# Performance work log

Measured on AMD Instinct MI355X. Metric: run time of the kernel, lower is better.

Reference implementation:

```python
import jax, jax.numpy as jnp
import numpy as np

N_NODES = 50000
N_EDGES = 800000
HID = 256
HEADS = 4
HEAD_C = HID // HEADS  # 64
IN_CH = 16
OUT_CH = 4
NEG_SLOPE = 0.2  # PyG GATConv default LeakyReLU slope
LN_EPS = 1e-5


def setup_inputs() -> dict:
    key = jax.random.key(0)
    ks = jax.random.split(key, 12)
    s = 0.05
    return {
        "x": jax.random.normal(ks[0], (N_NODES, IN_CH), dtype=jnp.float32),
        "edge_index": jax.random.randint(ks[1], (2, N_EDGES), 0, N_NODES, dtype=jnp.int64),
        "w_in": jax.random.normal(ks[2], (IN_CH, HID), dtype=jnp.float32) * s,
        "b_in": jnp.zeros((HID,), dtype=jnp.float32),
        "w_gat": jax.random.normal(ks[3], (4, HID, HID), dtype=jnp.float32) * s,
        "att_src": jax.random.normal(ks[4], (4, HEADS, HEAD_C), dtype=jnp.float32) * s,
        "att_dst": jax.random.normal(ks[5], (4, HEADS, HEAD_C), dtype=jnp.float32) * s,
        "b_gat": jnp.zeros((4, HID), dtype=jnp.float32),
        "ln_scale": jnp.ones((4, HID), dtype=jnp.float32),
        "ln_bias": jnp.zeros((4, HID), dtype=jnp.float32),
        "w_out": jax.random.normal(ks[6], (HID, OUT_CH), dtype=jnp.float32) * s,
        "b_out": jnp.zeros((OUT_CH,), dtype=jnp.float32),
    }


def _gat_layer(x, src, dst, W, a_src, a_dst, bias, g, beta):
    """One GATConv(concat, heads=4) + LayerNorm + ELU. x:[N,HID]."""
    n = x.shape[0]
    h = (x @ W).reshape(n, HEADS, HEAD_C)                 # [N,H,C]
    a_s = jnp.einsum("nhc,hc->nh", h, a_src)              # [N,H]
    a_d = jnp.einsum("nhc,hc->nh", h, a_dst)              # [N,H]
    logits = jax.nn.leaky_relu(a_s[src] + a_d[dst], NEG_SLOPE)  # [E,H]
    # segment softmax over destination neighborhoods (self-loops ensure non-empty)
    m = jax.ops.segment_max(logits, dst, num_segments=n)
    e = jnp.exp(logits - m[dst])
    denom = jax.ops.segment_sum(e, dst, num_segments=n)
    alpha = e / (denom[dst] + 1e-16)                      # [E,H]
    msg = alpha[:, :, None] * h[src]                      # [E,H,C]
    out = jax.ops.segment_sum(msg, dst, num_segments=n).reshape(n, HID) + bias
    mu = out.mean(-1, keepdims=True)
    var = out.var(-1, keepdims=True)
    out = (out - mu) * jax.lax.rsqrt(var + LN_EPS) * g + beta
    return jax.nn.elu(out)


def reference(x, edge_index, w_in, b_in, w_gat, att_src, att_dst, b_gat,
              ln_scale, ln_bias, w_out, b_out):
    n = x.shape[0]
    # PyG GATConv adds self-loops by default
    loops = jnp.arange(n, dtype=edge_index.dtype)
    ei = jnp.concatenate([edge_index, jnp.stack([loops, loops])], axis=1)
    src, dst = ei[0], ei[1]

    x = x @ w_in + b_in                                   # input_proj
    h = x
    for l in (0, 1):
        h = _gat_layer(h, src, dst, w_gat[l], att_src[l], att_dst[l],
                       b_gat[l], ln_scale[l], ln_bias[l])
    x = x + h
    h = x
    for l in (2, 3):
        h = _gat_layer(h, src, dst, w_gat[l], att_src[l], att_dst[l],
                       b_gat[l], ln_scale[l], ln_bias[l])
    x = x + h
    return x @ w_out + b_out
```

## Files before the change

### kernel.cpp

```cpp
#include <hip/hip_runtime.h>
#include <math.h>

#define NN 50000
#define E0 800000
#define ET 850000
#define HID 256
#define INCH 16
#define MAXDEG 64

typedef _Float16 h8 __attribute__((ext_vector_type(8)));
typedef float f32x4 __attribute__((ext_vector_type(4)));

__global__ void scatter_pad_kernel(const int* __restrict__ ei, int* __restrict__ cursor,
                                   int* __restrict__ csr_pad) {
    int e = blockIdx.x * blockDim.x + threadIdx.x;
    if (e >= ET) return;
    int s, d;
    if (e < E0) { s = ei[e]; d = ei[E0 + e]; }
    else        { s = d = e - E0; }
    int pos = atomicAdd(&cursor[d], 1);
    if (pos < MAXDEG) csr_pad[(d << 6) + pos] = s;
}

__global__ __launch_bounds__(256) void wt_kernel(const float* __restrict__ w,
                                                 _Float16* __restrict__ wt) {
    int k = blockIdx.x, l = blockIdx.y, n = threadIdx.x;
    float v = w[((size_t)l * 256 + k) * 256 + n];
    wt[((size_t)l * 256 + n) * 256 + k] = (_Float16)v;
}

__global__ __launch_bounds__(256) void input_proj_kernel(
    const float* __restrict__ x, const float* __restrict__ w,
    const float* __restrict__ b, _Float16* __restrict__ outh) {
    int n = blockIdx.x, j = threadIdx.x;
    __shared__ float xs[INCH];
    if (j < INCH) xs[j] = x[n * INCH + j];
    __syncthreads();
    float acc = b[j];
#pragma unroll
    for (int k = 0; k < INCH; k++) acc += xs[k] * w[k * HID + j];
    outh[n * HID + j] = (_Float16)acc;
}

__global__ __launch_bounds__(512) void gemm_fused_kernel(
    const _Float16* __restrict__ A, const _Float16* __restrict__ BT,
    _Float16* __restrict__ H, const float* __restrict__ att_s,
    const float* __restrict__ att_d, float* __restrict__ AS, float* __restrict__ AD,
    int N) {
    int t = threadIdx.x;
    int wv = t >> 6, lane = t & 63;
    int rb = blockIdx.x * 128;
    int wr = (wv >> 2) * 64, wc = (wv & 3) * 64;
    int lm = lane & 15, lq = lane >> 4;
    f32x4 acc[4][4] = {};

    const _Float16* ap[4];
#pragma unroll
    for (int i = 0; i < 4; ++i) {
        int ra = rb + wr + i * 16 + lm;
        if (ra >= N) ra = N - 1;
        ap[i] = A + (size_t)ra * 256 + lq * 8;
    }
    const _Float16* bp[4];
#pragma unroll
    for (int j = 0; j < 4; ++j)
        bp[j] = BT + (size_t)(wc + j * 16 + lm) * 256 + lq * 8;

#pragma unroll 2
    for (int k0 = 0; k0 < 256; k0 += 32) {
        h8 af[4], bfr[4];
#pragma unroll
        for (int i = 0; i < 4; ++i) af[i] = *(const h8*)(ap[i] + k0);
#pragma unroll
        for (int j = 0; j < 4; ++j) bfr[j] = *(const h8*)(bp[j] + k0);
#pragma unroll
        for (int i = 0; i < 4; ++i)
#pragma unroll
            for (int j = 0; j < 4; ++j)
                acc[i][j] = __builtin_amdgcn_mfma_f32_16x16x32_f16(af[i], bfr[j], acc[i][j], 0, 0, 0);
    }

    int head = wv & 3;
    float sa[4], sd[4];
#pragma unroll
    for (int j = 0; j < 4; ++j) {
        sa[j] = att_s[head * 64 + j * 16 + lm];
        sd[j] = att_d[head * 64 + j * 16 + lm];
    }
#pragma unroll
    for (int i = 0; i < 4; ++i)
#pragma unroll
        for (int rr = 0; rr < 4; ++rr) {
            float vs = acc[i][0][rr] * sa[0] + acc[i][1][rr] * sa[1]
                     + acc[i][2][rr] * sa[2] + acc[i][3][rr] * sa[3];
            float vd = acc[i][0][rr] * sd[0] + acc[i][1][rr] * sd[1]
                     + acc[i][2][rr] * sd[2] + acc[i][3][rr] * sd[3];
#pragma unroll
            for (int o = 1; o <= 8; o <<= 1) {
                vs += __shfl_xor(vs, o, 64);
                vd += __shfl_xor(vd, o, 64);
            }
            int row = rb + wr + i * 16 + lq * 4 + rr;
            if (lm == 0 && row < N) {
                AS[row * 4 + head] = vs;
                AD[row * 4 + head] = vd;
            }
        }

#pragma unroll
    for (int i = 0; i < 4; ++i)
#pragma unroll
        for (int j = 0; j < 4; ++j) {
            int col = wc + j * 16 + lm;
#pragma unroll
            for (int rr = 0; rr < 4; ++rr) {
                int row = rb + wr + i * 16 + lq * 4 + rr;
                if (row < N) H[(size_t)row * 256 + col] = (_Float16)acc[i][j][rr];
            }
        }
}

__global__ __launch_bounds__(256) void agg_kernel(
    const _Float16* __restrict__ H, const float4* __restrict__ AS,
    const float4* __restrict__ AD,
    const int* __restrict__ cnt, const int* __restrict__ csr_pad,
    const float* __restrict__ bias, const float* __restrict__ g, const float* __restrict__ beta,
    const _Float16* __restrict__ res, _Float16* __restrict__ outh) {
    int t = threadIdx.x;
    int l32 = t & 31;
    int n = blockIdx.x * 8 + (t >> 5);
    int deg = cnt[n];
    if (deg > MAXDEG) deg = MAXDEG;
    int start = n << 6, end = start + deg;
    float4 adv = AD[n];
    int head = l32 >> 3;
    int c0 = l32 * 8;
    float advh = (head == 0) ? adv.x : (head == 1) ? adv.y : (head == 2) ? adv.z : adv.w;

    float acc[8] = {};
    float acc_e = 0.f;
#pragma unroll 4
    for (int i = start; i < end; ++i) {
        int s = csr_pad[i];
        const float* as = (const float*)&AS[s];
        float v = as[head] + advh;
        v = (v >= 0.f) ? v : 0.2f * v;
        float e = __expf(v);
        acc_e += e;
        h8 hv = *(const h8*)(H + (size_t)s * 256 + c0);
#pragma unroll
        for (int k = 0; k < 8; ++k) acc[k] += e * (float)hv[k];
    }
    float dinv = 1.f / (acc_e + 1e-16f);

    float val[8];
#pragma unroll
    for (int k = 0; k < 8; k += 4) {
        float4 bb = *(const float4*)(bias + c0 + k);
        val[k]     = acc[k]     * dinv + bb.x;
        val[k + 1] = acc[k + 1] * dinv + bb.y;
        val[k + 2] = acc[k + 2] * dinv + bb.z;
        val[k + 3] = acc[k + 3] * dinv + bb.w;
    }

    float s1 = 0.f, s2 = 0.f;
#pragma unroll
    for (int k = 0; k < 8; ++k) { s1 += val[k]; s2 += val[k] * val[k]; }
#pragma unroll
    for (int o = 16; o >= 1; o >>= 1) {
        s1 += __shfl_xor(s1, o, 64);
        s2 += __shfl_xor(s2, o, 64);
    }
    float mu = s1 * (1.f / 256.f);
    float var = s2 * (1.f / 256.f) - mu * mu;
    float rs = rsqrtf(var + 1e-5f);

    float y[8];
#pragma unroll
    for (int k = 0; k < 8; k += 4) {
        float4 g4 = *(const float4*)(g + c0 + k);
        float4 b4 = *(const float4*)(beta + c0 + k);
        y[k]     = (val[k]     - mu) * rs * g4.x + b4.x;
        y[k + 1] = (val[k + 1] - mu) * rs * g4.y + b4.y;
        y[k + 2] = (val[k + 2] - mu) * rs * g4.z + b4.z;
        y[k + 3] = (val[k + 3] - mu) * rs * g4.w + b4.w;
    }
#pragma unroll
    for (int k = 0; k < 8; ++k) y[k] = (y[k] > 0.f) ? y[k] : (__expf(y[k]) - 1.f);
    if (res) {
        h8 r0 = *(const h8*)(res + (size_t)n * 256 + c0);
#pragma unroll
        for (int k = 0; k < 8; ++k) y[k] += (float)r0[k];
    }
    h8 o0;
#pragma unroll
    for (int k = 0; k < 8; ++k) o0[k] = (_Float16)y[k];
    *(h8*)(outh + (size_t)n * 256 + c0) = o0;
}

__global__ __launch_bounds__(256) void out_proj_kernel(
    const _Float16* __restrict__ x, const float* __restrict__ w,
    const float* __restrict__ b, float* __restrict__ out, int n) {
    int tid = blockIdx.x * blockDim.x + threadIdx.x;
    int node = tid >> 6, lane = tid & 63;
    if (node >= n) return;
    const _Float16* xp = x + (size_t)node * HID + lane * 4;
    float x0 = (float)xp[0], x1 = (float)xp[1], x2 = (float)xp[2], x3 = (float)xp[3];
    const float4* wr = (const float4*)w;
    float4 w0 = wr[lane * 4 + 0];
    float4 w1 = wr[lane * 4 + 1];
    float4 w2 = wr[lane * 4 + 2];
    float4 w3 = wr[lane * 4 + 3];
    float o0 = x0 * w0.x + x1 * w1.x + x2 * w2.x + x3 * w3.x;
    float o1 = x0 * w0.y + x1 * w1.y + x2 * w2.y + x3 * w3.y;
    float o2 = x0 * w0.z + x1 * w1.z + x2 * w2.z + x3 * w3.z;
    float o3 = x0 * w0.w + x1 * w1.w + x2 * w2.w + x3 * w3.w;
#pragma unroll
    for (int o = 32; o >= 1; o >>= 1) {
        o0 += __shfl_down(o0, o, 64);
        o1 += __shfl_down(o1, o, 64);
        o2 += __shfl_down(o2, o, 64);
        o3 += __shfl_down(o3, o, 64);
    }
    if (lane == 0) {
        out[node * 4 + 0] = o0 + b[0];
        out[node * 4 + 1] = o1 + b[1];
        out[node * 4 + 2] = o2 + b[2];
        out[node * 4 + 3] = o3 + b[3];
    }
}

extern "C" void kernel_launch(void* const* d_in, const int* in_sizes, int n_in,
                              void* d_out, int out_size, void* d_ws, size_t ws_size,
                              hipStream_t stream) {
    const float* x       = (const float*)d_in[0];
    const int*   ei      = (const int*)  d_in[1];
    const float* w_in    = (const float*)d_in[2];
    const float* b_in    = (const float*)d_in[3];
    const float* w_gat   = (const float*)d_in[4];
    const float* att_src = (const float*)d_in[5];
    const float* att_dst = (const float*)d_in[6];
    const float* b_gat   = (const float*)d_in[7];
    const float* ln_g    = (const float*)d_in[8];
    const float* ln_b    = (const float*)d_in[9];
    const float* w_out   = (const float*)d_in[10];
    const float* b_out   = (const float*)d_in[11];
    float* out = (float*)d_out;

    char* ws = (char*)d_ws;
    size_t off = 0;
    auto alloc = [&](size_t bytes) {
        void* p = ws + off;
        off += (bytes + 255) & ~(size_t)255;
        return p;
    };
    _Float16*  Ph      = (_Float16*)alloc((size_t)NN * HID * 2);
    _Float16*  Ch      = (_Float16*)alloc((size_t)NN * HID * 2);
    _Float16*  Gh      = (_Float16*)alloc((size_t)NN * HID * 2);
    _Float16*  H       = (_Float16*)alloc((size_t)NN * HID * 2);
    _Float16*  WT      = (_Float16*)alloc((size_t)4 * HID * HID * 2);
    float*     ASAD    = (float*)alloc((size_t)NN * 8 * 4);
    int*       cursor  = (int*)alloc((size_t)NN * 4);
    int*       csr_pad = (int*)alloc((size_t)NN * MAXDEG * 4);

    float* AS = ASAD;
    float* AD = ASAD + (size_t)NN * 4;

    const int NB_EDGE = (ET + 255) / 256;
    const int NB_GEMM = (NN + 127) / 128;
    const int NB_AGG = NN / 8;

    hipMemsetAsync(cursor, 0, (size_t)NN * 4, stream);
    scatter_pad_kernel<<<NB_EDGE, 256, 0, stream>>>(ei, cursor, csr_pad);

    wt_kernel<<<dim3(256, 4), 256, 0, stream>>>(w_gat, WT);
    input_proj_kernel<<<NN, 256, 0, stream>>>(x, w_in, b_in, Ph);

    auto run_layer = [&](const _Float16* inh, int l, const _Float16* res, _Float16* outh) {
        gemm_fused_kernel<<<NB_GEMM, 512, 0, stream>>>(
            inh, WT + (size_t)l * HID * HID, H,
            att_src + l * 256, att_dst + l * 256, AS, AD, NN);
        agg_kernel<<<NB_AGG, 256, 0, stream>>>(
            H, (const float4*)AS, (const float4*)AD, cursor, csr_pad,
            b_gat + l * 256, ln_g + l * 256, ln_b + l * 256, res, outh);
    };

    run_layer(Ph, 0, nullptr, Gh);
    run_layer(Gh, 1, Ph,      Ch);
    run_layer(Ch, 2, nullptr, Gh);
    run_layer(Gh, 3, Ch,      Ph);

    out_proj_kernel<<<(NN * 64 + 255) / 256, 256, 0, stream>>>(Ph, w_out, b_out, out, NN);
}
```

Before: 616.1 us.

## Fuse prep kernels and stage GEMM tiles through swizzled LDS

Merges the edge scatter, weight transpose and input projection into one prep kernel, and vectorises the input projection so 32 threads handle one node with 8 outputs each. The GEMM moves from 512-thread blocks covering all 256 columns, which read fragments straight from global memory, to a 2D grid of 256-thread blocks with 128x128 tiles. These tiles are staged through XOR-swizzled LDS using global_load_lds. The goal is fewer launches and better operand reuse and coalescing. In exchange, the GEMM adds per-k-step barriers with no double buffering, and each block now sees only two heads.

```diff
diff --git a/kernel.cpp b/kernel.cpp
--- a/kernel.cpp
+++ b/kernel.cpp
@@ -8,79 +8,118 @@
 #define INCH 16
 #define MAXDEG 64
 
+#define NB_EDGE 3321
+#define NB_WT   256
+#define NB_IP   6250
+#define NB_PREP (NB_EDGE + NB_WT + NB_IP)
+
 typedef _Float16 h8 __attribute__((ext_vector_type(8)));
 typedef float f32x4 __attribute__((ext_vector_type(4)));
 
-__global__ void scatter_pad_kernel(const int* __restrict__ ei, int* __restrict__ cursor,
-                                   int* __restrict__ csr_pad) {
-    int e = blockIdx.x * blockDim.x + threadIdx.x;
-    if (e >= ET) return;
-    int s, d;
-    if (e < E0) { s = ei[e]; d = ei[E0 + e]; }
-    else        { s = d = e - E0; }
-    int pos = atomicAdd(&cursor[d], 1);
-    if (pos < MAXDEG) csr_pad[(d << 6) + pos] = s;
-}
-
-__global__ __launch_bounds__(256) void wt_kernel(const float* __restrict__ w,
-                                                 _Float16* __restrict__ wt) {
-    int k = blockIdx.x, l = blockIdx.y, n = threadIdx.x;
-    float v = w[((size_t)l * 256 + k) * 256 + n];
-    wt[((size_t)l * 256 + n) * 256 + k] = (_Float16)v;
-}
-
-__global__ __launch_bounds__(256) void input_proj_kernel(
-    const float* __restrict__ x, const float* __restrict__ w,
-    const float* __restrict__ b, _Float16* __restrict__ outh) {
-    int n = blockIdx.x, j = threadIdx.x;
-    __shared__ float xs[INCH];
-    if (j < INCH) xs[j] = x[n * INCH + j];
-    __syncthreads();
-    float acc = b[j];
-#pragma unroll
-    for (int k = 0; k < INCH; k++) acc += xs[k] * w[k * HID + j];
-    outh[n * HID + j] = (_Float16)acc;
-}
-
-__global__ __launch_bounds__(512) void gemm_fused_kernel(
+__device__ __forceinline__ void load_lds16(const void* g, void* l) {
+    __builtin_amdgcn_global_load_lds(
+        (const __attribute__((address_space(1))) unsigned int*)g,
+        (__attribute__((address_space(3))) unsigned int*)l, 16, 0, 0);
+}
+
+__global__ __launch_bounds__(256) void prep_kernel(
+    const int* __restrict__ ei, int* __restrict__ cursor, int* __restrict__ csr_pad,
+    const float* __restrict__ w_gat, _Float16* __restrict__ WT,
+    const float* __restrict__ x, const float* __restrict__ w_in,
+    const float* __restrict__ b_in, _Float16* __restrict__ Ph) {
+    int b = blockIdx.x, t = threadIdx.x;
+    if (b < NB_EDGE) {
+        int e = b * 256 + t;
+        if (e < ET) {
+            int s, d;
+            if (e < E0) { s = ei[e]; d = ei[E0 + e]; }
+            else        { s = d = e - E0; }
+            int pos = atomicAdd(&cursor[d], 1);
+            if (pos < MAXDEG) csr_pad[(d << 6) + pos] = s;
+        }
+    } else if (b < NB_EDGE + NB_WT) {
+        int k = b - NB_EDGE;
+#pragma unroll
+        for (int l = 0; l < 4; ++l) {
+            float v = w_gat[((size_t)l * 256 + k) * 256 + t];
+            WT[((size_t)l * 256 + t) * 256 + k] = (_Float16)v;
+        }
+    } else {
+        int ipb = b - NB_EDGE - NB_WT;
+        int sub = t >> 5, l32 = t & 31;
+        int n = ipb * 8 + sub;
+        int c0 = l32 * 8;
+        const float* xr = x + n * INCH;
+        float a[8];
+#pragma unroll
+        for (int k = 0; k < 8; k += 4) {
+            float4 bb = *(const float4*)(b_in + c0 + k);
+            a[k] = bb.x; a[k + 1] = bb.y; a[k + 2] = bb.z; a[k + 3] = bb.w;
+        }
+#pragma unroll
+        for (int k = 0; k < INCH; ++k) {
+            float xv = xr[k];
+            const float4 w0 = *(const float4*)(w_in + k * 256 + c0);
+            const float4 w1 = *(const float4*)(w_in + k * 256 + c0 + 4);
+            a[0] += xv * w0.x; a[1] += xv * w0.y; a[2] += xv * w0.z; a[3] += xv * w0.w;
+            a[4] += xv * w1.x; a[5] += xv * w1.y; a[6] += xv * w1.z; a[7] += xv * w1.w;
+        }
+        h8 o;
+#pragma unroll
+        for (int k = 0; k < 8; ++k) o[k] = (_Float16)a[k];
+        *(h8*)(Ph + (size_t)n * 256 + c0) = o;
+    }
+}
+
+__global__ __launch_bounds__(256) void gemm_fused_kernel(
     const _Float16* __restrict__ A, const _Float16* __restrict__ BT,
     _Float16* __restrict__ H, const float* __restrict__ att_s,
     const float* __restrict__ att_d, float* __restrict__ AS, float* __restrict__ AD,
     int N) {
+    __shared__ _Float16 As[128 * 32];
+    __shared__ _Float16 Bs[128 * 32];
     int t = threadIdx.x;
     int wv = t >> 6, lane = t & 63;
-    int rb = blockIdx.x * 128;
-    int wr = (wv >> 2) * 64, wc = (wv & 3) * 64;
+    int rb = blockIdx.x * 128, cb = blockIdx.y * 128;
+    int wr = (wv >> 1) * 64, wc = (wv & 1) * 64;
     int lm = lane & 15, lq = lane >> 4;
     f32x4 acc[4][4] = {};
 
-    const _Float16* ap[4];
-#pragma unroll
-    for (int i = 0; i < 4; ++i) {
-        int ra = rb + wr + i * 16 + lm;
-        if (ra >= N) ra = N - 1;
-        ap[i] = A + (size_t)ra * 256 + lq * 8;
-    }
-    const _Float16* bp[4];
-#pragma unroll
-    for (int j = 0; j < 4; ++j)
-        bp[j] = BT + (size_t)(wc + j * 16 + lm) * 256 + lq * 8;
-
-#pragma unroll 2
+    int rch = lane >> 2;
+    int q = lane & 3;
+
     for (int k0 = 0; k0 < 256; k0 += 32) {
+#pragma unroll
+        for (int c = 0; c < 2; ++c) {
+            int r = wv * 32 + c * 16 + rch;
+            int g = q ^ (r & 3);
+            int ra = rb + r; if (ra >= N) ra = N - 1;
+            load_lds16(A + (size_t)ra * 256 + k0 + g * 8,
+                       (char*)As + wv * 2048 + c * 1024);
+            load_lds16(BT + (size_t)(cb + r) * 256 + k0 + g * 8,
+                       (char*)Bs + wv * 2048 + c * 1024);
+        }
+        __syncthreads();
         h8 af[4], bfr[4];
 #pragma unroll
-        for (int i = 0; i < 4; ++i) af[i] = *(const h8*)(ap[i] + k0);
-#pragma unroll
-        for (int j = 0; j < 4; ++j) bfr[j] = *(const h8*)(bp[j] + k0);
+        for (int i = 0; i < 4; ++i) {
+            int row = wr + i * 16 + lm;
+            af[i] = *(const h8*)((const char*)As + row * 64 + ((lq ^ (row & 3)) * 16));
+        }
+#pragma unroll
+        for (int j = 0; j < 4; ++j) {
+            int row = wc + j * 16 + lm;
+            bfr[j] = *(const h8*)((const char*)Bs + row * 64 + ((lq ^ (row & 3)) * 16));
+        }
 #pragma unroll
         for (int i = 0; i < 4; ++i)
 #pragma unroll
             for (int j = 0; j < 4; ++j)
                 acc[i][j] = __builtin_amdgcn_mfma_f32_16x16x32_f16(af[i], bfr[j], acc[i][j], 0, 0, 0);
-    }
-
-    int head = wv & 3;
+        __syncthreads();
+    }
+
+    int head = (cb + wc) >> 6;
     float sa[4], sd[4];
 #pragma unroll
     for (int j = 0; j < 4; ++j) {
@@ -111,7 +150,7 @@
     for (int i = 0; i < 4; ++i)
 #pragma unroll
         for (int j = 0; j < 4; ++j) {
-            int col = wc + j * 16 + lm;
+            int col = cb + wc + j * 16 + lm;
 #pragma unroll
             for (int rr = 0; rr < 4; ++rr) {
                 int row = rb + wr + i * 16 + lq * 4 + rr;
@@ -266,18 +305,15 @@
     float* AS = ASAD;
     float* AD = ASAD + (size_t)NN * 4;
 
-    const int NB_EDGE = (ET + 255) / 256;
-    const int NB_GEMM = (NN + 127) / 128;
+    const dim3 GEMM_GRID((NN + 127) / 128, 2);
     const int NB_AGG = NN / 8;
 
     hipMemsetAsync(cursor, 0, (size_t)NN * 4, stream);
-    scatter_pad_kernel<<<NB_EDGE, 256, 0, stream>>>(ei, cursor, csr_pad);
-
-    wt_kernel<<<dim3(256, 4), 256, 0, stream>>>(w_gat, WT);
-    input_proj_kernel<<<NN, 256, 0, stream>>>(x, w_in, b_in, Ph);
+    prep_kernel<<<NB_PREP, 256, 0, stream>>>(ei, cursor, csr_pad, w_gat, WT,
+                                             x, w_in, b_in, Ph);
 
     auto run_layer = [&](const _Float16* inh, int l, const _Float16* res, _Float16* outh) {
-        gemm_fused_kernel<<<NB_GEMM, 512, 0, stream>>>(
+        gemm_fused_kernel<<<GEMM_GRID, 256, 0, stream>>>(
             inh, WT + (size_t)l * HID * HID, H,
             att_src + l * 256, att_dst + l * 256, AS, AD, NN);
         agg_kernel<<<NB_AGG, 256, 0, stream>>>(
```

Measured after the change: 547.1 us. -11.2%, faster.
